# Kernel tuning notes

Measured on AMD Instinct MI355X. Metric: run time of the kernel, lower is better.

The kernel has to match this reference:

```python
import jax, jax.numpy as jnp
import numpy as np

N_NODES = 1048576   # total nodes across the ragged batch
N_GRAPHS = 16384    # number of graphs (segments)
D_IN = 128
D = 128


def setup_inputs() -> dict:
    key = jax.random.key(0)
    ks = jax.random.split(key, 8)
    x = jax.random.normal(ks[0], (N_NODES, D_IN), jnp.float32)
    graph_ids = jnp.sort(jax.random.randint(ks[1], (N_NODES,), 0, N_GRAPHS, jnp.int32))
    s_in = 1.0 / np.sqrt(D_IN)
    s_d = 1.0 / np.sqrt(D)
    W_enc = jax.random.normal(ks[2], (D_IN, D), jnp.float32) * s_in
    b_enc = jnp.zeros((D,), jnp.float32)
    w_q1 = jax.random.normal(ks[3], (D,), jnp.float32) * s_d
    b_q1 = jnp.zeros((), jnp.float32)
    w_q2 = jax.random.normal(ks[4], (D,), jnp.float32) * s_d
    b_q2 = jnp.zeros((), jnp.float32)
    return {"x": x, "graph_ids": graph_ids, "W_enc": W_enc, "b_enc": b_enc,
            "w_q1": w_q1, "b_q1": b_q1, "w_q2": w_q2, "b_q2": b_q2}


def _attention_query(h, graph_ids, w, b):
    # per-node score -> segment-softmax -> weighted segment sum (== masked attention pooling)
    s = h @ w + b                                                   # [N]
    m = jax.ops.segment_max(s, graph_ids, num_segments=N_GRAPHS)    # [G]
    e = jnp.exp(s - m[graph_ids])                                   # [N]
    z = jax.ops.segment_sum(e, graph_ids, num_segments=N_GRAPHS)    # [G]
    a = e / jnp.maximum(z, 1e-12)[graph_ids]                        # [N]
    return jax.ops.segment_sum(a[:, None] * h, graph_ids, num_segments=N_GRAPHS)  # [G, D]


def reference(x, graph_ids, W_enc, b_enc, w_q1, b_q1, w_q2, b_q2):
    # encoder: per-node feature transform
    h = jax.nn.relu(x @ W_enc + b_enc)                              # [N, D]
    # keys: masked mean pooling == segment mean
    counts = jax.ops.segment_sum(jnp.ones((N_NODES,), h.dtype), graph_ids,
                                 num_segments=N_GRAPHS)             # [G]
    keys = jax.ops.segment_sum(h, graph_ids, num_segments=N_GRAPHS) / \
        jnp.maximum(counts, 1.0)[:, None]                           # [G, D]
    q1 = _attention_query(h, graph_ids, w_q1, b_q1)
    q2 = _attention_query(h, graph_ids, w_q2, b_q2)
    return (keys, q1, q2)
```

## Files before the change

### kernel.cpp

```cpp
#include <hip/hip_runtime.h>
#include <hip/hip_bf16.h>

#define NN 1048576
#define NG 16384
#define DD 128
#define GRIDB 512
#define WPB 2
#define WSTRIDE (GRIDB * WPB)
#define RING 4

typedef __bf16 bf16x8 __attribute__((ext_vector_type(8)));
typedef float f32x4 __attribute__((ext_vector_type(4)));

__device__ __forceinline__ unsigned short f2bf(float f) {
    unsigned int u = __float_as_uint(f);
    u += 0x7FFFu + ((u >> 16) & 1u);
    return (unsigned short)(u >> 16);
}

__global__ void prep_kernel(const int* __restrict__ gid, const float* __restrict__ W,
                            int* __restrict__ starts, unsigned short* __restrict__ Wl) {
    int t = blockIdx.x * 256 + threadIdx.x;
    if (t <= NG) {
        int lo = 0, hi = NN;
        while (lo < hi) { int mid = (lo + hi) >> 1; if (gid[mid] < t) lo = mid + 1; else hi = mid; }
        starts[t] = lo;
    }
    if (t < DD * DD) {
        int e = t & 7, l = (t >> 3) & 63, kk = (t >> 9) & 3, n = t >> 11;
        int k = kk * 32 + (l >> 4) * 8 + e;
        int col = n * 16 + (l & 15);
        Wl[t] = f2bf(W[k * DD + col]);
    }
}

__global__ __launch_bounds__(128, 1) void fused_kernel(
    const float* __restrict__ x, const int* __restrict__ starts,
    const unsigned short* __restrict__ Wl,
    const float* __restrict__ b_enc, const float* __restrict__ w_q1,
    const float* __restrict__ b_q1, const float* __restrict__ w_q2,
    const float* __restrict__ b_q2, float* __restrict__ out) {

    __shared__ float xbuf[WPB][RING][16 * 128];

    const int t = threadIdx.x, w = t >> 6, l = t & 63;
    const int lr = l & 15, lk = l >> 4;

    bf16x8 wfr[8][4];
#pragma unroll
    for (int n = 0; n < 8; ++n)
#pragma unroll
        for (int kk = 0; kk < 4; ++kk)
            wfr[n][kk] = *(const bf16x8*)&Wl[((n * 4 + kk) * 64 + l) * 8];

    float br[8], w1r[8], w2r[8];
#pragma unroll
    for (int n = 0; n < 8; ++n) {
        br[n]  = b_enc[n * 16 + lr];
        w1r[n] = w_q1[n * 16 + lr];
        w2r[n] = w_q2[n * 16 + lr];
    }
    const float bq1 = b_q1[0], bq2 = b_q2[0];

    const int p = blockIdx.x * WPB + w;

    int ig = p;
    int ic0 = starts[ig], is1 = starts[ig + 1];
    while (ic0 >= is1) {
        ig += WSTRIDE;
        if (ig >= NG) break;
        ic0 = starts[ig]; is1 = starts[ig + 1];
    }

    auto issue_tile = [&](int bufIdx) {
        const int hi = is1 - 1;
#pragma unroll
        for (int inst = 0; inst < 8; ++inst) {
            const int rit = inst * 2 + (l >> 5);
            const int grow = min(ic0 + rit, hi);
            const int su = (l & 31) ^ (rit & 7);
            const float* src = x + (size_t)grow * DD + su * 4;
            float* dst = &xbuf[w][bufIdx][inst * 256];
            __builtin_amdgcn_global_load_lds(
                (const __attribute__((address_space(1))) void*)src,
                (__attribute__((address_space(3))) void*)dst, 16, 0, 0);
        }
    };
    auto adv_issue = [&]() {
        ic0 += 16;
        while (ic0 >= is1) {
            ig += WSTRIDE;
            if (ig >= NG) break;
            ic0 = starts[ig]; is1 = starts[ig + 1];
        }
    };

    int inflight = 0;
#pragma unroll
    for (int r = 0; r < RING; ++r)
        if (ig < NG) { issue_tile(r); adv_issue(); inflight++; }
    int buf = 0;

    for (int cg = p; cg < NG; cg += WSTRIDE) {
        const int cs0 = starts[cg], cs1 = starts[cg + 1];
        const int cnt = cs1 - cs0;

        float m1 = -1e30f, m2 = -1e30f, z1 = 0.f, z2 = 0.f;
        float ka[8], q1a[8], q2a[8];
#pragma unroll
        for (int n = 0; n < 8; ++n) { ka[n] = 0.f; q1a[n] = 0.f; q2a[n] = 0.f; }

        for (int cc0 = cs0; cc0 < cs1; cc0 += 16) {
            switch (inflight) {
                case 4: asm volatile("s_waitcnt vmcnt(24)" ::: "memory"); break;
                case 3: asm volatile("s_waitcnt vmcnt(16)" ::: "memory"); break;
                case 2: asm volatile("s_waitcnt vmcnt(8)"  ::: "memory"); break;
                default: asm volatile("s_waitcnt vmcnt(0)" ::: "memory"); break;
            }

            const float* xb = &xbuf[w][buf][0];
            bf16x8 afr[4];
#pragma unroll
            for (int kk = 0; kk < 4; ++kk) {
                const int u0 = (kk * 8 + lk * 2)     ^ (lr & 7);
                const int u1 = (kk * 8 + lk * 2 + 1) ^ (lr & 7);
                const float4 f0 = *(const float4*)&xb[lr * 128 + u0 * 4];
                const float4 f1 = *(const float4*)&xb[lr * 128 + u1 * 4];
                bf16x8 a;
                a[0] = (__bf16)f0.x; a[1] = (__bf16)f0.y; a[2] = (__bf16)f0.z; a[3] = (__bf16)f0.w;
                a[4] = (__bf16)f1.x; a[5] = (__bf16)f1.y; a[6] = (__bf16)f1.z; a[7] = (__bf16)f1.w;
                afr[kk] = a;
            }
            asm volatile("s_waitcnt lgkmcnt(0)" ::: "memory");
            inflight--;
            if (ig < NG) { issue_tile(buf); adv_issue(); inflight++; }
            buf = (buf + 1) & (RING - 1);

            f32x4 acc[8];
#pragma unroll
            for (int n = 0; n < 8; ++n) { acc[n][0] = 0.f; acc[n][1] = 0.f; acc[n][2] = 0.f; acc[n][3] = 0.f; }
#pragma unroll
            for (int n = 0; n < 8; ++n)
#pragma unroll
                for (int kk = 0; kk < 4; ++kk)
                    acc[n] = __builtin_amdgcn_mfma_f32_16x16x32_bf16(afr[kk], wfr[n][kk], acc[n], 0, 0, 0);

            float p1[4] = {0.f, 0.f, 0.f, 0.f}, p2[4] = {0.f, 0.f, 0.f, 0.f};
#pragma unroll
            for (int n = 0; n < 8; ++n) {
#pragma unroll
                for (int j = 0; j < 4; ++j) {
                    float hv = fmaxf(acc[n][j] + br[n], 0.f);
                    acc[n][j] = hv;
                    p1[j] += hv * w1r[n];
                    p2[j] += hv * w2r[n];
                }
            }
#pragma unroll
            for (int j = 0; j < 4; ++j)
#pragma unroll
                for (int d = 1; d < 16; d <<= 1) {
                    p1[j] += __shfl_xor(p1[j], d);
                    p2[j] += __shfl_xor(p2[j], d);
                }

            float v1[4], v2[4];
            float r1 = -1e30f, r2 = -1e30f;
#pragma unroll
            for (int j = 0; j < 4; ++j) {
                const bool vv = (cc0 + lk * 4 + j) < cs1;
                v1[j] = vv ? p1[j] + bq1 : -1e30f;
                v2[j] = vv ? p2[j] + bq2 : -1e30f;
                r1 = fmaxf(r1, v1[j]); r2 = fmaxf(r2, v2[j]);
            }
            r1 = fmaxf(r1, __shfl_xor(r1, 16)); r1 = fmaxf(r1, __shfl_xor(r1, 32));
            r2 = fmaxf(r2, __shfl_xor(r2, 16)); r2 = fmaxf(r2, __shfl_xor(r2, 32));

            const float nm1 = fmaxf(m1, r1), nm2 = fmaxf(m2, r2);
            const float sc1 = __expf(m1 - nm1), sc2 = __expf(m2 - nm2);
            float e1j[4], e2j[4];
            float cz1 = 0.f, cz2 = 0.f;
#pragma unroll
            for (int j = 0; j < 4; ++j) {
                e1j[j] = __expf(v1[j] - nm1);
                e2j[j] = __expf(v2[j] - nm2);
                cz1 += e1j[j]; cz2 += e2j[j];
            }
            cz1 += __shfl_xor(cz1, 16); cz1 += __shfl_xor(cz1, 32);
            cz2 += __shfl_xor(cz2, 16); cz2 += __shfl_xor(cz2, 32);
            z1 = z1 * sc1 + cz1; z2 = z2 * sc2 + cz2;
            m1 = nm1; m2 = nm2;

#pragma unroll
            for (int n = 0; n < 8; ++n) {
                float kaa = 0.f, q1aa = 0.f, q2aa = 0.f;
#pragma unroll
                for (int j = 0; j < 4; ++j) {
                    const float hv = acc[n][j];
                    const bool vv = (cc0 + lk * 4 + j) < cs1;
                    kaa  += vv ? hv : 0.f;
                    q1aa += e1j[j] * hv;
                    q2aa += e2j[j] * hv;
                }
                ka[n] += kaa;
                q1a[n] = q1a[n] * sc1 + q1aa;
                q2a[n] = q2a[n] * sc2 + q2aa;
            }
        }

#pragma unroll
        for (int n = 0; n < 8; ++n)
#pragma unroll
            for (int d = 16; d < 64; d <<= 1) {
                ka[n]  += __shfl_xor(ka[n],  d);
                q1a[n] += __shfl_xor(q1a[n], d);
                q2a[n] += __shfl_xor(q2a[n], d);
            }
        const float inv_cnt = 1.f / fmaxf((float)cnt, 1.f);
        const float iz1 = 1.f / fmaxf(z1, 1e-12f);
        const float iz2 = 1.f / fmaxf(z2, 1e-12f);
#pragma unroll
        for (int n2 = 0; n2 < 2; ++n2) {
            const int n = lk * 2 + n2;
            const int col = n * 16 + lr;
            out[(size_t)cg * DD + col]            = ka[n]  * inv_cnt;
            out[(size_t)(NG + cg) * DD + col]     = q1a[n] * iz1;
            out[(size_t)(2 * NG + cg) * DD + col] = q2a[n] * iz2;
        }
    }
}

extern "C" void kernel_launch(void* const* d_in, const int* in_sizes, int n_in,
                              void* d_out, int out_size, void* d_ws, size_t ws_size,
                              hipStream_t stream) {
    const float* x     = (const float*)d_in[0];
    const int*   gid   = (const int*)d_in[1];
    const float* W     = (const float*)d_in[2];
    const float* b_enc = (const float*)d_in[3];
    const float* w_q1  = (const float*)d_in[4];
    const float* b_q1  = (const float*)d_in[5];
    const float* w_q2  = (const float*)d_in[6];
    const float* b_q2  = (const float*)d_in[7];
    float* out = (float*)d_out;

    int* starts        = (int*)d_ws;
    unsigned short* Wl = (unsigned short*)((char*)d_ws + 131072);

    prep_kernel<<<65, 256, 0, stream>>>(gid, W, starts, Wl);
    fused_kernel<<<GRIDB, 128, 0, stream>>>(x, starts, Wl, b_enc, w_q1, b_q1, w_q2, b_q2, out);
}
```

Before: 203.4 us.

## Replace LDS-direct ring prefetch with register-staged double buffering, four waves per block

Async global_load_lds with a 4-deep ring and explicit vmcnt waits is replaced by register prefetch of the next tile into float4 registers, written into LDS double buffers after the current tile's fragments are read. The block grows from 2 to 4 waves, so 2048 waves cover the graphs instead of 1024. This trades prefetch depth (one tile ahead instead of up to four) and extra VGPRs for more wave-level parallelism and simpler synchronisation. There is no explicit wait or barrier between the LDS write and the later read, so correctness depends on compiler-inserted waitcnts, which should hold because each wave only uses its own buffers.

```diff
diff --git a/kernel.cpp b/kernel.cpp
--- a/kernel.cpp
+++ b/kernel.cpp
@@ -5,9 +5,7 @@
 #define NG 16384
 #define DD 128
 #define GRIDB 512
-#define WPB 2
-#define WSTRIDE (GRIDB * WPB)
-#define RING 4
+#define WSTRIDE (GRIDB * 4)
 
 typedef __bf16 bf16x8 __attribute__((ext_vector_type(8)));
 typedef float f32x4 __attribute__((ext_vector_type(4)));
@@ -34,14 +32,14 @@
     }
 }
 
-__global__ __launch_bounds__(128, 1) void fused_kernel(
+__global__ __launch_bounds__(256) void fused_kernel(
     const float* __restrict__ x, const int* __restrict__ starts,
     const unsigned short* __restrict__ Wl,
     const float* __restrict__ b_enc, const float* __restrict__ w_q1,
     const float* __restrict__ b_q1, const float* __restrict__ w_q2,
     const float* __restrict__ b_q2, float* __restrict__ out) {
 
-    __shared__ float xbuf[WPB][RING][16 * 128];
+    __shared__ float xbuf[4][2][16 * 128];
 
     const int t = threadIdx.x, w = t >> 6, l = t & 63;
     const int lr = l & 15, lk = l >> 4;
@@ -62,7 +60,7 @@
     }
     const float bq1 = b_q1[0], bq2 = b_q2[0];
 
-    const int p = blockIdx.x * WPB + w;
+    const int p = blockIdx.x * 4 + w;
 
     int ig = p;
     int ic0 = starts[ig], is1 = starts[ig + 1];
@@ -72,18 +70,23 @@
         ic0 = starts[ig]; is1 = starts[ig + 1];
     }
 
-    auto issue_tile = [&](int bufIdx) {
+    float4 pf[8];
+
+    auto load_pf = [&]() {
         const int hi = is1 - 1;
 #pragma unroll
-        for (int inst = 0; inst < 8; ++inst) {
-            const int rit = inst * 2 + (l >> 5);
-            const int grow = min(ic0 + rit, hi);
-            const int su = (l & 31) ^ (rit & 7);
-            const float* src = x + (size_t)grow * DD + su * 4;
-            float* dst = &xbuf[w][bufIdx][inst * 256];
-            __builtin_amdgcn_global_load_lds(
-                (const __attribute__((address_space(1))) void*)src,
-                (__attribute__((address_space(3))) void*)dst, 16, 0, 0);
+        for (int i = 0; i < 8; ++i) {
+            const int r = i * 2 + (l >> 5);
+            const int grow = min(ic0 + r, hi);
+            pf[i] = *(const float4*)(x + (size_t)grow * DD + (l & 31) * 4);
+        }
+    };
+    auto stage_write = [&](int b) {
+#pragma unroll
+        for (int i = 0; i < 8; ++i) {
+            const int r = i * 2 + (l >> 5);
+            const int u = (l & 31) ^ (r & 7);
+            *(float4*)&xbuf[w][b][r * 128 + u * 4] = pf[i];
         }
     };
     auto adv_issue = [&]() {
@@ -95,10 +98,11 @@
         }
     };
 
-    int inflight = 0;
-#pragma unroll
-    for (int r = 0; r < RING; ++r)
-        if (ig < NG) { issue_tile(r); adv_issue(); inflight++; }
+    bool pfv = false;
+    if (ig < NG) {
+        load_pf(); adv_issue(); stage_write(0);
+        if (ig < NG) { load_pf(); adv_issue(); pfv = true; }
+    }
     int buf = 0;
 
     for (int cg = p; cg < NG; cg += WSTRIDE) {
@@ -111,13 +115,6 @@
         for (int n = 0; n < 8; ++n) { ka[n] = 0.f; q1a[n] = 0.f; q2a[n] = 0.f; }
 
         for (int cc0 = cs0; cc0 < cs1; cc0 += 16) {
-            switch (inflight) {
-                case 4: asm volatile("s_waitcnt vmcnt(24)" ::: "memory"); break;
-                case 3: asm volatile("s_waitcnt vmcnt(16)" ::: "memory"); break;
-                case 2: asm volatile("s_waitcnt vmcnt(8)"  ::: "memory"); break;
-                default: asm volatile("s_waitcnt vmcnt(0)" ::: "memory"); break;
-            }
-
             const float* xb = &xbuf[w][buf][0];
             bf16x8 afr[4];
 #pragma unroll
@@ -131,10 +128,10 @@
                 a[4] = (__bf16)f1.x; a[5] = (__bf16)f1.y; a[6] = (__bf16)f1.z; a[7] = (__bf16)f1.w;
                 afr[kk] = a;
             }
-            asm volatile("s_waitcnt lgkmcnt(0)" ::: "memory");
-            inflight--;
-            if (ig < NG) { issue_tile(buf); adv_issue(); inflight++; }
-            buf = (buf + 1) & (RING - 1);
+
+            if (pfv) stage_write(buf ^ 1);
+            if (ig < NG) { load_pf(); adv_issue(); pfv = true; } else pfv = false;
+            buf ^= 1;
 
             f32x4 acc[8];
 #pragma unroll
@@ -247,5 +244,5 @@
     unsigned short* Wl = (unsigned short*)((char*)d_ws + 131072);
 
     prep_kernel<<<65, 256, 0, stream>>>(gid, W, starts, Wl);
-    fused_kernel<<<GRIDB, 128, 0, stream>>>(x, starts, Wl, b_enc, w_q1, b_q1, w_q2, b_q2, out);
-}
+    fused_kernel<<<GRIDB, 256, 0, stream>>>(x, starts, Wl, b_enc, w_q1, b_q1, w_q2, b_q2, out);
+}
```

Result: slower. 613.7 us (+201.6%).
